# Performance work log

Measured on AMD Instinct MI355X. Metric: run time of the kernel, lower is better.

## Reference

```python
import jax, jax.numpy as jnp
import numpy as np

C_IN, C_OUT = 256, 128
D_STATE, D_CONV, EXPAND = 16, 4, 2
D_INNER = EXPAND * C_OUT            # 256
DT_RANK = (C_OUT + 15) // 16        # 8
EPS = 1e-5


def setup_inputs() -> dict:
    key = jax.random.key(0)
    ks = jax.random.split(key, 20)
    n = lambda k, s, sc=0.02: (sc * jax.random.normal(k, s)).astype(jnp.float32)
    inp = jax.random.normal(ks[0], (2, C_IN, 32, 32), dtype=jnp.float32)
    skip = jax.random.normal(ks[1], (2, C_OUT, 64, 64), dtype=jnp.float32)
    # ConvTranspose2d weight: [in, out, kh, kw], k=2, stride=2, pad=0 (get_padding(2,2)=0), out_pad=0
    w_up = n(ks[2], (C_IN, C_OUT, 2, 2))
    # fuse: transposed 1x1 stride 1 == plain 1x1; torch weight [in=2*C_OUT, out=C_OUT]
    w_fuse = n(ks[3], (2 * C_OUT, C_OUT))
    # mixer projections
    gW_in = n(ks[4], (C_OUT, C_OUT))
    gW_gate = n(ks[5], (C_OUT, C_OUT))
    gb_gate = jnp.zeros((C_OUT,), jnp.float32)
    ln_g = jnp.ones((C_OUT,), jnp.float32)
    ln_b = jnp.zeros((C_OUT,), jnp.float32)
    gW_out = n(ks[6], (C_OUT, C_OUT))
    # Mamba params
    m_Win = n(ks[7], (2 * D_INNER, C_OUT))
    m_convw = n(ks[8], (D_INNER, 1, D_CONV), 0.1)
    m_convb = jnp.zeros((D_INNER,), jnp.float32)
    m_Wx = n(ks[9], (DT_RANK + 2 * D_STATE, D_INNER))
    m_Wdt = n(ks[10], (D_INNER, DT_RANK), 0.1)
    m_bdt = jnp.full((D_INNER,), -2.0, jnp.float32)
    m_Alog = jnp.broadcast_to(jnp.log(jnp.arange(1, D_STATE + 1, dtype=jnp.float32)), (D_INNER, D_STATE)).copy()
    m_D = jnp.ones((D_INNER,), jnp.float32)
    m_Wout = n(ks[11], (C_OUT, D_INNER))
    return dict(inp=inp, skip=skip, w_up=w_up, w_fuse=w_fuse, gW_in=gW_in, gW_gate=gW_gate,
                gb_gate=gb_gate, ln_g=ln_g, ln_b=ln_b, gW_out=gW_out, m_Win=m_Win,
                m_convw=m_convw, m_convb=m_convb, m_Wx=m_Wx, m_Wdt=m_Wdt, m_bdt=m_bdt,
                m_Alog=m_Alog, m_D=m_D, m_Wout=m_Wout)


def _instance_norm(x):  # [B,C,H,W], affine=False (MONAI default)
    mu = jnp.mean(x, axis=(2, 3), keepdims=True)
    var = jnp.var(x, axis=(2, 3), keepdims=True)
    return (x - mu) * jax.lax.rsqrt(var + EPS)


def _layernorm(x, g, b):  # over last dim
    mu = jnp.mean(x, axis=-1, keepdims=True)
    var = jnp.var(x, axis=-1, keepdims=True)
    return (x - mu) * jax.lax.rsqrt(var + EPS) * g + b


def _mamba(t, m_Win, m_convw, m_convb, m_Wx, m_Wdt, m_bdt, m_Alog, m_D, m_Wout):
    # t: [B, L, C]
    B, L, _ = t.shape
    xz = jnp.einsum('blc,ec->ble', t, m_Win)              # [B,L,2*dI]
    xm, zm = jnp.split(xz, 2, axis=-1)                    # [B,L,dI] each
    # depthwise causal conv along L
    xc = jax.lax.conv_general_dilated(
        xm.transpose(0, 2, 1), m_convw, window_strides=(1,),
        padding=((D_CONV - 1, 0),), feature_group_count=D_INNER,
        dimension_numbers=('NCH', 'OIH', 'NCH'))
    xc = jax.nn.silu(xc.transpose(0, 2, 1) + m_convb)     # [B,L,dI]
    x_dbl = jnp.einsum('bld,ed->ble', xc, m_Wx)           # [B,L,dt_rank+2*dS]
    dt = jax.nn.softplus(jnp.einsum('blr,dr->bld', x_dbl[..., :DT_RANK], m_Wdt) + m_bdt)
    Bm = x_dbl[..., DT_RANK:DT_RANK + D_STATE]            # [B,L,dS]
    Cm = x_dbl[..., DT_RANK + D_STATE:]                   # [B,L,dS]
    A = -jnp.exp(m_Alog)                                  # [dI,dS]
    dA = jnp.exp(dt[..., None] * A)                       # [B,L,dI,dS]
    dBx = (dt * xc)[..., None] * Bm[:, :, None, :]        # [B,L,dI,dS]

    def step(h, io):
        dA_t, dBx_t, C_t = io
        h = dA_t * h + dBx_t                              # [B,dI,dS]
        y = jnp.einsum('bds,bs->bd', h, C_t)
        return h, y

    h0 = jnp.zeros((B, D_INNER, D_STATE), t.dtype)
    _, ys = jax.lax.scan(step, h0, (dA.transpose(1, 0, 2, 3), dBx.transpose(1, 0, 2, 3), Cm.transpose(1, 0, 2)))
    y = ys.transpose(1, 0, 2) + xc * m_D
    y = y * jax.nn.silu(zm)
    return jnp.einsum('bld,cd->blc', y, m_Wout)


def _mixer(x, gW_in, gW_gate, gb_gate, ln_g, ln_b, gW_out,
           m_Win, m_convw, m_convb, m_Wx, m_Wdt, m_bdt, m_Alog, m_D, m_Wout):
    B, C, H, W = x.shape
    tokens = x.transpose(0, 2, 3, 1).reshape(B, H * W, C)
    tokens = jnp.einsum('blc,oc->blo', tokens, gW_in)
    z = jax.nn.sigmoid(jax.nn.silu(jnp.einsum('blc,oc->blo', tokens, gW_gate) + gb_gate))
    t = _layernorm(tokens, ln_g, ln_b)
    y = _mamba(t, m_Win, m_convw, m_convb, m_Wx, m_Wdt, m_bdt, m_Alog, m_D, m_Wout)
    out = tokens + jnp.einsum('blc,oc->blo', y * z, gW_out)
    return out.reshape(B, H, W, C).transpose(0, 3, 1, 2)


def reference(inp, skip, w_up, w_fuse, gW_in, gW_gate, gb_gate, ln_g, ln_b, gW_out,
              m_Win, m_convw, m_convb, m_Wx, m_Wdt, m_bdt, m_Alog, m_D, m_Wout):
    # transposed conv: k=2, stride=2, pad=0, out_pad=0 -> lhs_dilation trick
    kern = jnp.flip(w_up, (2, 3)).transpose(1, 0, 2, 3)   # [out,in,kh,kw]
    up = jax.lax.conv_general_dilated(
        inp, kern, window_strides=(1, 1), padding=((1, 1), (1, 1)),
        lhs_dilation=(2, 2), dimension_numbers=('NCHW', 'OIHW', 'NCHW'))  # [B,128,64,64]
    # spatial sizes match skip -> crop/pad is identity
    cat = jnp.concatenate([up, skip], axis=1)             # [B,256,64,64]
    fused = jnp.einsum('bihw,io->bohw', cat, w_fuse)      # 1x1 fuse
    x = jax.nn.leaky_relu(_instance_norm(fused), 0.01)
    mix = _mixer(x, gW_in, gW_gate, gb_gate, ln_g, ln_b, gW_out,
                 m_Win, m_convw, m_convb, m_Wx, m_Wdt, m_bdt, m_Alog, m_D, m_Wout)
    out = x + mix
    return _instance_norm(out)
```

## Files before the change

kernel.cpp:

```cpp
#include <hip/hip_runtime.h>
#include <math.h>

#define BB 2
#define CIN 256
#define COUT 128
#define LL 4096
#define DI 256
#define DS 16

#define SC_T 16
#define SC_NC 256
#define SXP 260
#define NSUP 16
#define CPS 16

#define L2E 1.44269504088896340736f
#define LN2 0.69314718055994530942f

__device__ __forceinline__ float ex2_(float x){ return __builtin_amdgcn_exp2f(x); }
__device__ __forceinline__ float fexp_(float x){ return ex2_(x * L2E); }
__device__ __forceinline__ float rcp_(float x){ return __builtin_amdgcn_rcpf(x); }
__device__ __forceinline__ float silu_(float x){ return x * rcp_(1.f + fexp_(-x)); }
__device__ __forceinline__ float sigm_(float x){ return rcp_(1.f + fexp_(-x)); }
__device__ __forceinline__ float softplus_(float x){
  return (x > 20.f) ? x : LN2 * __builtin_amdgcn_logf(1.f + fexp_(x));
}

__global__ __launch_bounds__(256) void k_weff(const float* __restrict__ w_up,
                       const float* __restrict__ w_fuse, float* __restrict__ W_eff){
  int idx = blockIdx.x * 256 + threadIdx.x;
  int o = idx & 127;
  int c = (idx >> 7) & 255;
  int p = idx >> 15;
  int kh = p >> 1, kw = p & 1;
  float acc = 0.f;
  #pragma unroll 8
  for (int i = 0; i < COUT; ++i)
    acc += w_up[((c * COUT + i) * 2 + kh) * 2 + kw] * w_fuse[i * COUT + o];
  W_eff[idx] = acc;
}

__global__ __launch_bounds__(256) void k_tr_all(
    const float* __restrict__ gW_in, const float* __restrict__ gW_gate,
    const float* __restrict__ gW_out, const float* __restrict__ m_Win,
    const float* __restrict__ m_Wout, const float* __restrict__ m_Alog,
    float* __restrict__ gW_inT, float* __restrict__ gW_gateT,
    float* __restrict__ gW_outT, float* __restrict__ m_WinT,
    float* __restrict__ m_WoutT, float* __restrict__ Aexp){
  int idx = blockIdx.x * 256 + threadIdx.x;
  if (idx < 16384){ int r = idx >> 7, c = idx & 127; gW_inT[c * 128 + r] = gW_in[idx]; }
  else if (idx < 32768){ int i = idx - 16384; int r = i >> 7, c = i & 127; gW_gateT[c * 128 + r] = gW_gate[i]; }
  else if (idx < 49152){ int i = idx - 32768; int r = i >> 7, c = i & 127; gW_outT[c * 128 + r] = gW_out[i]; }
  else if (idx < 114688){ int i = idx - 49152; int r = i >> 7, c = i & 127; m_WinT[c * 512 + r] = m_Win[i]; }
  else if (idx < 147456){ int i = idx - 114688; int r = i >> 8, c = i & 255; m_WoutT[c * 128 + r] = m_Wout[i]; }
  else if (idx < 151552){ int i = idx - 147456; Aexp[i] = -expf(m_Alog[i]) * L2E; }
}

__global__ __launch_bounds__(512, 8) void k_fused(const float* __restrict__ inp,
                        const float* __restrict__ skip,
                        const float* __restrict__ W_eff, const float* __restrict__ w_fuse,
                        float* __restrict__ fusedT, float* __restrict__ partials1){
  int bid = blockIdx.x;
  int wt = bid & 3;
  int h  = (bid >> 2) & 63;
  int b  = bid >> 8;
  int t  = threadIdx.x;
  int o  = t & 127;
  int g  = t >> 7;

  __shared__ float sIn[256 * 8];
  __shared__ float sSk[128 * 16];
  __shared__ float sS[512], sQ[512];
  int hi = h >> 1;
  int wi0 = wt * 8;
  #pragma unroll
  for (int k = 0; k < 4; ++k){
    int e = k * 512 + t;
    int c = e >> 3, wl = e & 7;
    sIn[e] = inp[((b * 256 + c) * 32 + hi) * 32 + wi0 + wl];
  }
  #pragma unroll
  for (int k = 0; k < 4; ++k){
    int e = k * 512 + t;
    int i = e >> 4, wl2 = e & 15;
    sSk[e] = skip[((b * 128 + i) * 64 + h) * 64 + wt * 16 + wl2];
  }
  __syncthreads();

  float acc[4];
  #pragma unroll
  for (int j = 0; j < 4; ++j) acc[j] = 0.f;

  for (int par = 0; par < 2; ++par){
    int p = (h & 1) * 2 + par;
    const float* wptr = W_eff + (size_t)p * 256 * 128 + o;
    for (int c = 0; c < 256; ++c){
      float we = wptr[c * 128];
      acc[par]     += sIn[c * 8 + g * 2]     * we;
      acc[2 + par] += sIn[c * 8 + g * 2 + 1] * we;
    }
  }
  for (int i = 0; i < 128; ++i){
    float wf = w_fuse[(128 + i) * 128 + o];
    #pragma unroll
    for (int j = 0; j < 4; ++j)
      acc[j] += sSk[i * 16 + g * 4 + j] * wf;
  }
  float s4 = 0.f, q4 = 0.f;
  #pragma unroll
  for (int j = 0; j < 4; ++j){
    int w = wt * 16 + g * 4 + j;
    fusedT[((size_t)(b * 4096 + h * 64 + w)) * 128 + o] = acc[j];
    s4 += acc[j]; q4 += acc[j] * acc[j];
  }
  sS[t] = s4; sQ[t] = q4;
  __syncthreads();
  if (t < 128){
    partials1[(size_t)bid * 256 + t * 2]     = sS[t] + sS[t + 128] + sS[t + 256] + sS[t + 384];
    partials1[(size_t)bid * 256 + t * 2 + 1] = sQ[t] + sQ[t + 128] + sQ[t + 256] + sQ[t + 384];
  }
}

__global__ __launch_bounds__(256) void k_stats2(const float* __restrict__ partials, int nb,
                         float cnt, float* __restrict__ mu, float* __restrict__ rs){
  int b = blockIdx.x;
  int t = threadIdx.x;
  int c = t & 127, half = t >> 7;
  int n2 = nb >> 1;
  float S = 0.f, Q = 0.f;
  for (int k = half * n2; k < (half + 1) * n2; ++k){
    S += partials[(size_t)(b * nb + k) * 256 + c * 2];
    Q += partials[(size_t)(b * nb + k) * 256 + c * 2 + 1];
  }
  __shared__ float sS[256], sQ[256];
  sS[t] = S; sQ[t] = Q;
  __syncthreads();
  if (t < 128){
    float Sa = sS[t] + sS[t + 128], Qa = sQ[t] + sQ[t + 128];
    float m = Sa / cnt;
    mu[b * 128 + t] = m;
    rs[b * 128 + t] = rsqrtf(Qa / cnt - m * m + 1e-5f);
  }
}

__global__ __launch_bounds__(512, 8) void k_front(const float* __restrict__ xt,
                      const float* __restrict__ mu1, const float* __restrict__ rs1,
                      const float* __restrict__ gW_inT, const float* __restrict__ gW_gateT,
                      const float* __restrict__ gb_gate,
                      const float* __restrict__ ln_g, const float* __restrict__ ln_b,
                      const float* __restrict__ m_WinT,
                      float* __restrict__ tok2, float* __restrict__ zb,
                      float* __restrict__ xm, float* __restrict__ zs){
  int tok0 = blockIdx.x * 8;
  int b = tok0 >> 12;
  int t = threadIdx.x;
  __shared__ float xn[128 * 8];
  __shared__ float tn[128 * 8];
  __shared__ float aT[8 * 132];
  __shared__ float sMu[8], sRs[8];

  #pragma unroll
  for (int k = 0; k < 2; ++k){
    int e = k * 512 + t;
    int tok = e >> 7, c = e & 127;
    float v = xt[(size_t)(tok0 + tok) * 128 + c];
    v = (v - mu1[b * 128 + c]) * rs1[b * 128 + c];
    v = v >= 0.f ? v : 0.01f * v;
    xn[c * 8 + tok] = v;
  }
  __syncthreads();

  int o = t & 127, th = t >> 7;
  float accA[2], accG[2];
  accA[0] = accA[1] = accG[0] = accG[1] = 0.f;
  for (int c = 0; c < 128; ++c){
    float wa = gW_inT[c * 128 + o];
    float wg = gW_gateT[c * 128 + o];
    float x0 = xn[c * 8 + th * 2], x1 = xn[c * 8 + th * 2 + 1];
    accA[0] += x0 * wa; accA[1] += x1 * wa;
    accG[0] += x0 * wg; accG[1] += x1 * wg;
  }
  float gb = gb_gate[o];
  #pragma unroll
  for (int j = 0; j < 2; ++j){
    int tok = th * 2 + j;
    tok2[(size_t)(tok0 + tok) * 128 + o] = accA[j];
    zb[(size_t)(tok0 + tok) * 128 + o] = sigm_(silu_(accG[j] + gb));
    aT[tok * 132 + o] = accA[j];
  }
  __syncthreads();

  if (t < 128){
    int tok = t >> 4, i = t & 15;
    float s = 0.f, q = 0.f;
    #pragma unroll
    for (int j = 0; j < 8; ++j){ float a = aT[tok * 132 + i * 8 + j]; s += a; q += a * a; }
    s += __shfl_down(s, 8, 16); q += __shfl_down(q, 8, 16);
    s += __shfl_down(s, 4, 16); q += __shfl_down(q, 4, 16);
    s += __shfl_down(s, 2, 16); q += __shfl_down(q, 2, 16);
    s += __shfl_down(s, 1, 16); q += __shfl_down(q, 1, 16);
    if (i == 0){
      float m = s / 128.f;
      sMu[tok] = m;
      sRs[tok] = rsqrtf(q / 128.f - m * m + 1e-5f);
    }
  }
  __syncthreads();
  #pragma unroll
  for (int k = 0; k < 2; ++k){
    int e = k * 512 + t;
    int tok = e >> 7, c = e & 127;
    tn[c * 8 + tok] = (aT[tok * 132 + c] - sMu[tok]) * sRs[tok] * ln_g[c] + ln_b[c];
  }
  __syncthreads();

  float a0[8];
  #pragma unroll
  for (int j = 0; j < 8; ++j) a0[j] = 0.f;
  for (int c = 0; c < 128; ++c){
    float w = m_WinT[c * 512 + t];
    float4 x0 = *(const float4*)&tn[c * 8];
    float4 x1 = *(const float4*)&tn[c * 8 + 4];
    a0[0] += x0.x * w; a0[1] += x0.y * w; a0[2] += x0.z * w; a0[3] += x0.w * w;
    a0[4] += x1.x * w; a0[5] += x1.y * w; a0[6] += x1.z * w; a0[7] += x1.w * w;
  }
  if (t < 256){
    #pragma unroll
    for (int j = 0; j < 8; ++j)
      xm[(size_t)(tok0 + j) * 256 + t] = a0[j];
  } else {
    #pragma unroll
    for (int j = 0; j < 8; ++j)
      zs[(size_t)(tok0 + j) * 256 + (t - 256)] = silu_(a0[j]);
  }
}

__global__ __launch_bounds__(1024, 8) void k_mid(const float* __restrict__ xm,
                    const float* __restrict__ cw, const float* __restrict__ cb,
                    const float* __restrict__ m_Wx, const float* __restrict__ m_Wdt,
                    const float* __restrict__ m_bdt, const float* __restrict__ Aexp,
                    float* __restrict__ xcb, float* __restrict__ dtb,
                    float* __restrict__ Bmb, float* __restrict__ Cmb,
                    float* __restrict__ chunkA, float* __restrict__ chunkH){
  int ch = blockIdx.x & (SC_NC - 1), b = blockIdx.x >> 8;
  int l0 = ch * SC_T;
  int tok0 = b * LL + l0;
  int t = threadIdx.x;
  __shared__ float sxc[SC_T * SXP];
  __shared__ float sdbl[SC_T * 40];

  {
    int d = t & 255, q = t >> 8;
    float xr[7];
    #pragma unroll
    for (int r = 0; r < 7; ++r){
      int l = l0 + q * 4 - 3 + r;
      xr[r] = (l >= 0) ? xm[(size_t)(b * LL + l) * 256 + d] : 0.f;
    }
    float4 cwv = *(const float4*)&cw[d * 4];
    float cbv = cb[d];
    #pragma unroll
    for (int j = 0; j < 4; ++j){
      float a = cbv + xr[j] * cwv.x + xr[j + 1] * cwv.y + xr[j + 2] * cwv.z + xr[j + 3] * cwv.w;
      a = silu_(a);
      int tok = q * 4 + j;
      sxc[tok * SXP + d] = a;
      xcb[(size_t)(tok0 + tok) * 256 + d] = a;
    }
  }
  __syncthreads();

  if (t < 512){
    int i = t & 31, tok = t >> 5;
    const float4* wrow = (const float4*)&m_Wx[(8 + i) * 256];
    const float4* xrow = (const float4*)&sxc[tok * SXP];
    float a0 = 0.f, a1 = 0.f, a2 = 0.f, a3 = 0.f;
    #pragma unroll 8
    for (int k = 0; k < 64; ++k){
      float4 w = wrow[k];
      float4 x = xrow[k];
      a0 += x.x * w.x; a1 += x.y * w.y; a2 += x.z * w.z; a3 += x.w * w.w;
    }
    float a = (a0 + a1) + (a2 + a3);
    sdbl[tok * 40 + 8 + i] = a;
    if (i < 16) Bmb[(size_t)(tok0 + tok) * 16 + i] = a;
    else        Cmb[(size_t)(tok0 + tok) * 16 + (i - 16)] = a;
  } else if (t < 640){
    int u = t - 512;
    int i = u & 7, tok = u >> 3;
    const float4* wrow = (const float4*)&m_Wx[i * 256];
    const float4* xrow = (const float4*)&sxc[tok * SXP];
    float a0 = 0.f, a1 = 0.f, a2 = 0.f, a3 = 0.f;
    #pragma unroll 8
    for (int k = 0; k < 64; ++k){
      float4 w = wrow[k];
      float4 x = xrow[k];
      a0 += x.x * w.x; a1 += x.y * w.y; a2 += x.z * w.z; a3 += x.w * w.w;
    }
    sdbl[tok * 40 + i] = (a0 + a1) + (a2 + a3);
  }
  __syncthreads();

  {
    int d = t & 255, sq = t >> 8;
    float4 wd0 = *(const float4*)&m_Wdt[d * 8];
    float4 wd1 = *(const float4*)&m_Wdt[d * 8 + 4];
    float bdt = m_bdt[d];
    float4 Av = *(const float4*)&Aexp[d * 16 + sq * 4];
    float A0 = Av.x, A1 = Av.y, A2 = Av.z, A3 = Av.w;
    float h0 = 0.f, h1 = 0.f, h2 = 0.f, h3 = 0.f;
    float sumdt = 0.f;
    #pragma unroll 2
    for (int j = 0; j < SC_T; ++j){
      const float4* dp = (const float4*)&sdbl[j * 40];
      float4 d0 = dp[0], d1 = dp[1];
      float dtr = bdt + d0.x * wd0.x + d0.y * wd0.y + d0.z * wd0.z + d0.w * wd0.w
                      + d1.x * wd1.x + d1.y * wd1.y + d1.z * wd1.z + d1.w * wd1.w;
      float dt = softplus_(dtr);
      if (sq == 0) dtb[(size_t)(tok0 + j) * 256 + d] = dt;
      sumdt += dt;
      float u = dt * sxc[j * SXP + d];
      float4 bv = *(const float4*)&sdbl[j * 40 + 8 + sq * 4];
      h0 = ex2_(dt * A0) * h0 + u * bv.x;
      h1 = ex2_(dt * A1) * h1 + u * bv.y;
      h2 = ex2_(dt * A2) * h2 + u * bv.z;
      h3 = ex2_(dt * A3) * h3 + u * bv.w;
    }
    size_t base = ((size_t)(b * SC_NC + ch)) * 4096 + d * 16 + sq * 4;
    float4 va, vh;
    va.x = ex2_(A0 * sumdt); va.y = ex2_(A1 * sumdt);
    va.z = ex2_(A2 * sumdt); va.w = ex2_(A3 * sumdt);
    vh.x = h0; vh.y = h1; vh.z = h2; vh.w = h3;
    *(float4*)&chunkA[base] = va;
    *(float4*)&chunkH[base] = vh;
  }
}

__global__ __launch_bounds__(256) void k_scanB1(const float* __restrict__ chunkA,
                        const float* __restrict__ chunkH,
                        float* __restrict__ superA, float* __restrict__ superH){
  int blk = blockIdx.x;
  int ds = (blk & 15) * 256 + threadIdx.x;
  int sc = (blk >> 4) & (NSUP - 1);
  int b  = blk >> 8;
  float sA = 1.f, sH = 0.f;
  for (int j = 0; j < CPS; ++j){
    size_t idx = ((size_t)(b * SC_NC + sc * CPS + j)) * 4096 + ds;
    float A = chunkA[idx], H = chunkH[idx];
    sA = A * sA;
    sH = A * sH + H;
  }
  size_t o = ((size_t)(b * NSUP + sc)) * 4096 + ds;
  superA[o] = sA; superH[o] = sH;
}

__global__ __launch_bounds__(256) void k_scanB2(const float* __restrict__ superA,
                        float* __restrict__ superH){
  int gid = blockIdx.x * 256 + threadIdx.x;
  int ds = gid & 4095;
  int b = gid >> 12;
  float carry = 0.f;
  #pragma unroll
  for (int sc = 0; sc < NSUP; ++sc){
    size_t idx = ((size_t)(b * NSUP + sc)) * 4096 + ds;
    float A = superA[idx], H = superH[idx];
    superH[idx] = carry;
    carry = A * carry + H;
  }
}

__global__ __launch_bounds__(256) void k_scanB3(const float* __restrict__ chunkA,
                        float* __restrict__ chunkH, const float* __restrict__ superH){
  int blk = blockIdx.x;
  int ds = (blk & 15) * 256 + threadIdx.x;
  int sc = (blk >> 4) & (NSUP - 1);
  int b  = blk >> 8;
  float carry = superH[((size_t)(b * NSUP + sc)) * 4096 + ds];
  for (int j = 0; j < CPS; ++j){
    size_t idx = ((size_t)(b * SC_NC + sc * CPS + j)) * 4096 + ds;
    float A = chunkA[idx], H = chunkH[idx];
    chunkH[idx] = carry;
    carry = A * carry + H;
  }
}

__global__ __launch_bounds__(1024, 8) void k_back(const float* __restrict__ dtb,
                        const float* __restrict__ xcb,
                        const float* __restrict__ Bmb, const float* __restrict__ Cmb,
                        const float* __restrict__ Aexp, const float* __restrict__ m_D,
                        const float* __restrict__ zs, const float* __restrict__ carryBuf,
                        const float* __restrict__ m_WoutT,
                        const float* __restrict__ zb, const float* __restrict__ gW_outT,
                        const float* __restrict__ xt, const float* __restrict__ tok2,
                        const float* __restrict__ mu1, const float* __restrict__ rs1,
                        float* __restrict__ outpre, float* __restrict__ partials2){
  int ch = blockIdx.x & (SC_NC - 1), b = blockIdx.x >> 8;
  int l0 = ch * SC_T;
  int tok0 = b * LL + l0;
  int t = threadIdx.x;
  __shared__ float sB[SC_T * 16], sC[SC_T * 16];
  __shared__ float yT[SC_T * 256];
  __shared__ float sv[SC_T * 128];
  __shared__ float sS[1024], sQ[1024];
  if (t < 256){
    sB[t] = Bmb[(size_t)tok0 * 16 + t];
    sC[t] = Cmb[(size_t)tok0 * 16 + t];
  }
  __syncthreads();

  {
    int sq = t & 3, d = t >> 2;
    float4 Av = *(const float4*)&Aexp[d * 16 + sq * 4];
    float A0 = Av.x, A1 = Av.y, A2 = Av.z, A3 = Av.w;
    size_t cbase = ((size_t)(b * SC_NC + ch)) * 4096 + d * 16 + sq * 4;
    float4 hv = *(const float4*)&carryBuf[cbase];
    float h0 = hv.x, h1 = hv.y, h2 = hv.z, h3 = hv.w;
    float Dv = m_D[d];
    const float* dtp = dtb + (size_t)tok0 * 256 + d;
    const float* xcp = xcb + (size_t)tok0 * 256 + d;
    const float* zp  = zs  + (size_t)tok0 * 256 + d;
    #pragma unroll 2
    for (int l = 0; l < SC_T; ++l){
      float dt = dtp[l * 256];
      float xc = xcp[l * 256];
      float u = dt * xc;
      float4 bv = *(const float4*)&sB[l * 16 + sq * 4];
      float4 cv = *(const float4*)&sC[l * 16 + sq * 4];
      h0 = ex2_(dt * A0) * h0 + u * bv.x;
      h1 = ex2_(dt * A1) * h1 + u * bv.y;
      h2 = ex2_(dt * A2) * h2 + u * bv.z;
      h3 = ex2_(dt * A3) * h3 + u * bv.w;
      float p = h0 * cv.x + h1 * cv.y + h2 * cv.z + h3 * cv.w;
      p += __shfl_xor(p, 1, 4);
      p += __shfl_xor(p, 2, 4);
      if (sq == 0){
        float zv = zp[l * 256];
        yT[l * 256 + d] = (p + xc * Dv) * zv;
      }
    }
  }
  __syncthreads();

  int cc = t & 127, th = t >> 7;
  float acc[2];
  acc[0] = acc[1] = 0.f;
  for (int dd = 0; dd < 256; ++dd){
    float w = m_WoutT[dd * 128 + cc];
    acc[0] += yT[(th * 2 + 0) * 256 + dd] * w;
    acc[1] += yT[(th * 2 + 1) * 256 + dd] * w;
  }
  #pragma unroll
  for (int j = 0; j < 2; ++j){
    int tok = th * 2 + j;
    float z = zb[(size_t)(tok0 + tok) * 128 + cc];
    sv[tok * 128 + cc] = acc[j] * z;
  }
  __syncthreads();

  float acc2[2];
  acc2[0] = acc2[1] = 0.f;
  for (int ci = 0; ci < 128; ++ci){
    float w = gW_outT[ci * 128 + cc];
    acc2[0] += sv[(th * 2 + 0) * 128 + ci] * w;
    acc2[1] += sv[(th * 2 + 1) * 128 + ci] * w;
  }
  float mu = mu1[b * 128 + cc], rsg = rs1[b * 128 + cc];
  float ps = 0.f, pq = 0.f;
  #pragma unroll
  for (int j = 0; j < 2; ++j){
    size_t idx = (size_t)(tok0 + th * 2 + j) * 128 + cc;
    float x = xt[idx];
    float xn = (x - mu) * rsg;
    xn = xn >= 0.f ? xn : 0.01f * xn;
    float v = xn + tok2[idx] + acc2[j];
    outpre[idx] = v;
    ps += v; pq += v * v;
  }
  sS[t] = ps; sQ[t] = pq;
  __syncthreads();
  if (t < 128){
    float S = 0.f, Q = 0.f;
    #pragma unroll
    for (int r = 0; r < 8; ++r){ S += sS[t + r * 128]; Q += sQ[t + r * 128]; }
    partials2[(size_t)blockIdx.x * 256 + t * 2]     = S;
    partials2[(size_t)blockIdx.x * 256 + t * 2 + 1] = Q;
  }
}

__global__ __launch_bounds__(256) void k_final(const float* __restrict__ outpre,
                        const float* __restrict__ mu,
                        const float* __restrict__ rs, float* __restrict__ out){
  int bid = blockIdx.x;
  int lg = bid & 127, cg = (bid >> 7) & 1, b = bid >> 8;
  int t = threadIdx.x;
  __shared__ float sT[64 * 33];
  int l0 = lg * 32, c0 = cg * 64;
  #pragma unroll
  for (int k = 0; k < 8; ++k){
    int e = k * 256 + t;
    int l = e >> 6, cc = e & 63;
    float v = outpre[(size_t)(b * 4096 + l0 + l) * 128 + c0 + cc];
    v = (v - mu[b * 128 + c0 + cc]) * rs[b * 128 + c0 + cc];
    sT[cc * 33 + l] = v;
  }
  __syncthreads();
  #pragma unroll
  for (int k = 0; k < 8; ++k){
    int e = k * 256 + t;
    int cc = e >> 5, l = e & 31;
    out[((size_t)(b * 128 + c0 + cc)) * 4096 + l0 + l] = sT[cc * 33 + l];
  }
}

extern "C" void kernel_launch(void* const* d_in, const int* in_sizes, int n_in,
                              void* d_out, int out_size, void* d_ws, size_t ws_size,
                              hipStream_t stream){
  const float* inp    = (const float*)d_in[0];
  const float* skip   = (const float*)d_in[1];
  const float* w_up   = (const float*)d_in[2];
  const float* w_fuse = (const float*)d_in[3];
  const float* gW_in  = (const float*)d_in[4];
  const float* gW_gate= (const float*)d_in[5];
  const float* gb_gate= (const float*)d_in[6];
  const float* ln_g   = (const float*)d_in[7];
  const float* ln_b   = (const float*)d_in[8];
  const float* gW_out = (const float*)d_in[9];
  const float* m_Win  = (const float*)d_in[10];
  const float* m_convw= (const float*)d_in[11];
  const float* m_convb= (const float*)d_in[12];
  const float* m_Wx   = (const float*)d_in[13];
  const float* m_Wdt  = (const float*)d_in[14];
  const float* m_bdt  = (const float*)d_in[15];
  const float* m_Alog = (const float*)d_in[16];
  const float* m_D    = (const float*)d_in[17];
  const float* m_Wout = (const float*)d_in[18];
  float* out = (float*)d_out;

  float* ws = (float*)d_ws;
  float* W_eff    = ws;
  float* xt       = W_eff + 131072;
  float* tok2     = xt + 1048576;
  float* zb       = tok2 + 1048576;
  float* xmbuf    = zb + 1048576;
  float* zs       = xmbuf + 2097152;
  float* xcb      = zs + 2097152;
  float* dtb      = xcb + 2097152;
  float* Bmb      = dtb + 2097152;
  float* Cmb      = Bmb + 131072;
  float* chunkA   = Cmb + 131072;
  float* chunkH   = chunkA + 2097152;
  float* superA   = chunkH + 2097152;
  float* superH   = superA + 131072;
  float* partials = superH + 131072;
  float* stats    = partials + 131072;
  float* gW_inT   = stats + 1024;
  float* gW_gateT = gW_inT + 16384;
  float* gW_outT  = gW_gateT + 16384;
  float* m_WinT   = gW_outT + 16384;
  float* m_WoutT  = m_WinT + 65536;
  float* AexpBuf  = m_WoutT + 32768;

  float* mu1 = stats, *rs1 = stats + 256, *mu2 = stats + 512, *rs2 = stats + 768;
  float* xm = xmbuf;
  float* outpre = xmbuf;

  k_weff<<<512, 256, 0, stream>>>(w_up, w_fuse, W_eff);
  k_tr_all<<<592, 256, 0, stream>>>(gW_in, gW_gate, gW_out, m_Win, m_Wout, m_Alog,
                                    gW_inT, gW_gateT, gW_outT, m_WinT, m_WoutT, AexpBuf);

  k_fused<<<512, 512, 0, stream>>>(inp, skip, W_eff, w_fuse, xt, partials);
  k_stats2<<<2, 256, 0, stream>>>(partials, 256, 4096.f, mu1, rs1);

  k_front<<<1024, 512, 0, stream>>>(xt, mu1, rs1, gW_inT, gW_gateT, gb_gate, ln_g, ln_b,
                                    m_WinT, tok2, zb, xm, zs);
  k_mid<<<512, 1024, 0, stream>>>(xm, m_convw, m_convb, m_Wx, m_Wdt, m_bdt, AexpBuf,
                                  xcb, dtb, Bmb, Cmb, chunkA, chunkH);
  k_scanB1<<<512, 256, 0, stream>>>(chunkA, chunkH, superA, superH);
  k_scanB2<<<32, 256, 0, stream>>>(superA, superH);
  k_scanB3<<<512, 256, 0, stream>>>(chunkA, chunkH, superH);
  k_back<<<512, 1024, 0, stream>>>(dtb, xcb, Bmb, Cmb, AexpBuf, m_D, zs, chunkH,
                                   m_WoutT, zb, gW_outT, xt, tok2, mu1, rs1,
                                   outpre, partials);
  k_stats2<<<2, 256, 0, stream>>>(partials, 256, 4096.f, mu2, rs2);
  k_final<<<512, 256, 0, stream>>>(outpre, mu2, rs2, out);
}
```

Before: 248.7 us.

## Merge prep kernels, precompute dt in k_mid, fold chunk carry fixup into k_back

Combines the W_eff and weight-transpose kernels into a single launch. In k_mid, dt is now computed once per token and shared through LDS, so the four state-quarter threads no longer each recompute the dt projection and softplus. The k_scanB3 pass is dropped: each k_back block rebuilds its own carry-in by scanning from the super-chunk carry across earlier chunks in its super-chunk. That removes a launch and a read-modify-write of chunkH, but adds redundant serial work of up to 15 steps per block in k_back.

```diff
diff --git a/kernel.cpp b/kernel.cpp
--- a/kernel.cpp
+++ b/kernel.cpp
@@ -26,34 +26,36 @@
   return (x > 20.f) ? x : LN2 * __builtin_amdgcn_logf(1.f + fexp_(x));
 }
 
-__global__ __launch_bounds__(256) void k_weff(const float* __restrict__ w_up,
-                       const float* __restrict__ w_fuse, float* __restrict__ W_eff){
-  int idx = blockIdx.x * 256 + threadIdx.x;
-  int o = idx & 127;
-  int c = (idx >> 7) & 255;
-  int p = idx >> 15;
-  int kh = p >> 1, kw = p & 1;
-  float acc = 0.f;
-  #pragma unroll 8
-  for (int i = 0; i < COUT; ++i)
-    acc += w_up[((c * COUT + i) * 2 + kh) * 2 + kw] * w_fuse[i * COUT + o];
-  W_eff[idx] = acc;
-}
-
-__global__ __launch_bounds__(256) void k_tr_all(
+__global__ __launch_bounds__(256) void k_prep(
+    const float* __restrict__ w_up, const float* __restrict__ w_fuse,
     const float* __restrict__ gW_in, const float* __restrict__ gW_gate,
     const float* __restrict__ gW_out, const float* __restrict__ m_Win,
     const float* __restrict__ m_Wout, const float* __restrict__ m_Alog,
+    float* __restrict__ W_eff,
     float* __restrict__ gW_inT, float* __restrict__ gW_gateT,
     float* __restrict__ gW_outT, float* __restrict__ m_WinT,
     float* __restrict__ m_WoutT, float* __restrict__ Aexp){
-  int idx = blockIdx.x * 256 + threadIdx.x;
-  if (idx < 16384){ int r = idx >> 7, c = idx & 127; gW_inT[c * 128 + r] = gW_in[idx]; }
-  else if (idx < 32768){ int i = idx - 16384; int r = i >> 7, c = i & 127; gW_gateT[c * 128 + r] = gW_gate[i]; }
-  else if (idx < 49152){ int i = idx - 32768; int r = i >> 7, c = i & 127; gW_outT[c * 128 + r] = gW_out[i]; }
-  else if (idx < 114688){ int i = idx - 49152; int r = i >> 7, c = i & 127; m_WinT[c * 512 + r] = m_Win[i]; }
-  else if (idx < 147456){ int i = idx - 114688; int r = i >> 8, c = i & 255; m_WoutT[c * 128 + r] = m_Wout[i]; }
-  else if (idx < 151552){ int i = idx - 147456; Aexp[i] = -expf(m_Alog[i]) * L2E; }
+  int bid = blockIdx.x;
+  if (bid < 512){
+    int idx = bid * 256 + threadIdx.x;
+    int o = idx & 127;
+    int c = (idx >> 7) & 255;
+    int p = idx >> 15;
+    int kh = p >> 1, kw = p & 1;
+    float acc = 0.f;
+    #pragma unroll 8
+    for (int i = 0; i < COUT; ++i)
+      acc += w_up[((c * COUT + i) * 2 + kh) * 2 + kw] * w_fuse[i * COUT + o];
+    W_eff[idx] = acc;
+  } else {
+    int idx = (bid - 512) * 256 + threadIdx.x;
+    if (idx < 16384){ int r = idx >> 7, c = idx & 127; gW_inT[c * 128 + r] = gW_in[idx]; }
+    else if (idx < 32768){ int i = idx - 16384; int r = i >> 7, c = i & 127; gW_gateT[c * 128 + r] = gW_gate[i]; }
+    else if (idx < 49152){ int i = idx - 32768; int r = i >> 7, c = i & 127; gW_outT[c * 128 + r] = gW_out[i]; }
+    else if (idx < 114688){ int i = idx - 49152; int r = i >> 7, c = i & 127; m_WinT[c * 512 + r] = m_Win[i]; }
+    else if (idx < 147456){ int i = idx - 114688; int r = i >> 8, c = i & 255; m_WoutT[c * 128 + r] = m_Wout[i]; }
+    else if (idx < 151552){ int i = idx - 147456; Aexp[i] = -expf(m_Alog[i]) * L2E; }
+  }
 }
 
 __global__ __launch_bounds__(512, 8) void k_fused(const float* __restrict__ inp,
@@ -247,6 +249,7 @@
   int tok0 = b * LL + l0;
   int t = threadIdx.x;
   __shared__ float sxc[SC_T * SXP];
+  __shared__ float sdt[SC_T * 256];
   __shared__ float sdbl[SC_T * 40];
 
   {
@@ -302,22 +305,34 @@
   __syncthreads();
 
   {
-    int d = t & 255, sq = t >> 8;
+    int d = t & 255;
     float4 wd0 = *(const float4*)&m_Wdt[d * 8];
     float4 wd1 = *(const float4*)&m_Wdt[d * 8 + 4];
     float bdt = m_bdt[d];
+    int tq = t >> 8;
+    #pragma unroll
+    for (int k = 0; k < 4; ++k){
+      int tok = k * 4 + tq;
+      const float4* dp = (const float4*)&sdbl[tok * 40];
+      float4 d0 = dp[0], d1 = dp[1];
+      float dtr = bdt + d0.x * wd0.x + d0.y * wd0.y + d0.z * wd0.z + d0.w * wd0.w
+                      + d1.x * wd1.x + d1.y * wd1.y + d1.z * wd1.z + d1.w * wd1.w;
+      float dt = softplus_(dtr);
+      sdt[tok * 256 + d] = dt;
+      dtb[(size_t)(tok0 + tok) * 256 + d] = dt;
+    }
+  }
+  __syncthreads();
+
+  {
+    int d = t & 255, sq = t >> 8;
     float4 Av = *(const float4*)&Aexp[d * 16 + sq * 4];
     float A0 = Av.x, A1 = Av.y, A2 = Av.z, A3 = Av.w;
     float h0 = 0.f, h1 = 0.f, h2 = 0.f, h3 = 0.f;
     float sumdt = 0.f;
-    #pragma unroll 2
+    #pragma unroll 4
     for (int j = 0; j < SC_T; ++j){
-      const float4* dp = (const float4*)&sdbl[j * 40];
-      float4 d0 = dp[0], d1 = dp[1];
-      float dtr = bdt + d0.x * wd0.x + d0.y * wd0.y + d0.z * wd0.z + d0.w * wd0.w
-                      + d1.x * wd1.x + d1.y * wd1.y + d1.z * wd1.z + d1.w * wd1.w;
-      float dt = softplus_(dtr);
-      if (sq == 0) dtb[(size_t)(tok0 + j) * 256 + d] = dt;
+      float dt = sdt[j * 256 + d];
       sumdt += dt;
       float u = dt * sxc[j * SXP + d];
       float4 bv = *(const float4*)&sdbl[j * 40 + 8 + sq * 4];
@@ -369,26 +384,13 @@
   }
 }
 
-__global__ __launch_bounds__(256) void k_scanB3(const float* __restrict__ chunkA,
-                        float* __restrict__ chunkH, const float* __restrict__ superH){
-  int blk = blockIdx.x;
-  int ds = (blk & 15) * 256 + threadIdx.x;
-  int sc = (blk >> 4) & (NSUP - 1);
-  int b  = blk >> 8;
-  float carry = superH[((size_t)(b * NSUP + sc)) * 4096 + ds];
-  for (int j = 0; j < CPS; ++j){
-    size_t idx = ((size_t)(b * SC_NC + sc * CPS + j)) * 4096 + ds;
-    float A = chunkA[idx], H = chunkH[idx];
-    chunkH[idx] = carry;
-    carry = A * carry + H;
-  }
-}
-
 __global__ __launch_bounds__(1024, 8) void k_back(const float* __restrict__ dtb,
                         const float* __restrict__ xcb,
                         const float* __restrict__ Bmb, const float* __restrict__ Cmb,
                         const float* __restrict__ Aexp, const float* __restrict__ m_D,
-                        const float* __restrict__ zs, const float* __restrict__ carryBuf,
+                        const float* __restrict__ zs,
+                        const float* __restrict__ chunkA, const float* __restrict__ chunkH,
+                        const float* __restrict__ superH,
                         const float* __restrict__ m_WoutT,
                         const float* __restrict__ zb, const float* __restrict__ gW_outT,
                         const float* __restrict__ xt, const float* __restrict__ tok2,
@@ -410,11 +412,21 @@
 
   {
     int sq = t & 3, d = t >> 2;
-    float4 Av = *(const float4*)&Aexp[d * 16 + sq * 4];
-    float A0 = Av.x, A1 = Av.y, A2 = Av.z, A3 = Av.w;
-    size_t cbase = ((size_t)(b * SC_NC + ch)) * 4096 + d * 16 + sq * 4;
-    float4 hv = *(const float4*)&carryBuf[cbase];
+    int ds4 = d * 16 + sq * 4;
+    float4 Av4 = *(const float4*)&Aexp[ds4];
+    float A0 = Av4.x, A1 = Av4.y, A2 = Av4.z, A3 = Av4.w;
+    int sc = ch >> 4;
+    float4 hv = *(const float4*)&superH[((size_t)(b * NSUP + sc)) * 4096 + ds4];
     float h0 = hv.x, h1 = hv.y, h2 = hv.z, h3 = hv.w;
+    for (int c2 = sc * CPS; c2 < ch; ++c2){
+      size_t ci = ((size_t)(b * SC_NC + c2)) * 4096 + ds4;
+      float4 cA = *(const float4*)&chunkA[ci];
+      float4 cH = *(const float4*)&chunkH[ci];
+      h0 = cA.x * h0 + cH.x;
+      h1 = cA.y * h1 + cH.y;
+      h2 = cA.z * h2 + cH.z;
+      h3 = cA.w * h3 + cH.w;
+    }
     float Dv = m_D[d];
     const float* dtp = dtb + (size_t)tok0 * 256 + d;
     const float* xcp = xcb + (size_t)tok0 * 256 + d;
@@ -564,9 +576,9 @@
   float* xm = xmbuf;
   float* outpre = xmbuf;
 
-  k_weff<<<512, 256, 0, stream>>>(w_up, w_fuse, W_eff);
-  k_tr_all<<<592, 256, 0, stream>>>(gW_in, gW_gate, gW_out, m_Win, m_Wout, m_Alog,
-                                    gW_inT, gW_gateT, gW_outT, m_WinT, m_WoutT, AexpBuf);
+  k_prep<<<1104, 256, 0, stream>>>(w_up, w_fuse, gW_in, gW_gate, gW_out, m_Win, m_Wout,
+                                   m_Alog, W_eff, gW_inT, gW_gateT, gW_outT, m_WinT,
+                                   m_WoutT, AexpBuf);
 
   k_fused<<<512, 512, 0, stream>>>(inp, skip, W_eff, w_fuse, xt, partials);
   k_stats2<<<2, 256, 0, stream>>>(partials, 256, 4096.f, mu1, rs1);
@@ -577,8 +589,8 @@
                                   xcb, dtb, Bmb, Cmb, chunkA, chunkH);
   k_scanB1<<<512, 256, 0, stream>>>(chunkA, chunkH, superA, superH);
   k_scanB2<<<32, 256, 0, stream>>>(superA, superH);
-  k_scanB3<<<512, 256, 0, stream>>>(chunkA, chunkH, superH);
-  k_back<<<512, 1024, 0, stream>>>(dtb, xcb, Bmb, Cmb, AexpBuf, m_D, zs, chunkH,
+  k_back<<<512, 1024, 0, stream>>>(dtb, xcb, Bmb, Cmb, AexpBuf, m_D, zs,
+                                   chunkA, chunkH, superH,
                                    m_WoutT, zb, gW_outT, xt, tok2, mu1, rs1,
                                    outpre, partials);
   k_stats2<<<2, 256, 0, stream>>>(partials, 256, 4096.f, mu2, rs2);
```

New measurement: 256.1 us. 1.03x slower.
